# Performance work log

Hardware: AMD Instinct MI355X
Metric: run time of the kernel (lower is better)

Reference implementation:

```python
import jax, jax.numpy as jnp
import numpy as np

GAMMA = 0.99
NUM_QUANTILES = 50
STEP_TYPE_LAST = 2
HUBER_DELTA = 1.0

T, B, Q = 128, 512, NUM_QUANTILES


def setup_inputs() -> dict:
    key = jax.random.key(0)
    k1, k2, k3, k4, k5 = jax.random.split(key, 5)
    return {
        "reward": jax.random.normal(k1, (T, B), dtype=jnp.float32),
        "step_type": jax.random.randint(k2, (T, B), 0, 3, dtype=jnp.int32),
        "discount": jax.random.uniform(k3, (T, B), dtype=jnp.float32),
        "value": jax.random.normal(k4, (T, B, Q), dtype=jnp.float32),
        "target_value": jax.random.normal(k5, (T, B, Q), dtype=jnp.float32),
    }


def discounted_return(rewards, values, step_types, discounts):
    """alf value_ops.discounted_return: backward-in-time recurrence.

    rewards/step_types/discounts: [T, B]; values: [T, B, Q].
    Returns [T-1, B, Q]. rets[T-1]=values[T-1];
    rets[t] = is_last[t]*values[t] + (1-is_last[t])*(discounts[t+1]*rets[t+1] + rewards[t+1]).
    """
    is_last = (step_types == STEP_TYPE_LAST).astype(values.dtype)[..., None]  # [T,B,1]
    r = rewards[..., None]    # [T,B,1]
    d = discounts[..., None]  # [T,B,1]

    def step(carry, xs):
        is_last_t, v_t, r_tp1, d_tp1 = xs
        acc = carry * d_tp1 + r_tp1
        ret = is_last_t * v_t + (1.0 - is_last_t) * acc
        return ret, ret

    init = values[-1]
    xs = (is_last[:-1], values[:-1], r[1:], d[1:])
    _, rets = jax.lax.scan(step, init, xs, reverse=True)
    return rets  # [T-1, B, Q]


def huber(x):
    ax = jnp.abs(x)
    return jnp.where(ax <= HUBER_DELTA, 0.5 * x * x, HUBER_DELTA * (ax - 0.5 * HUBER_DELTA))


def reference(reward, step_type, discount, value, target_value):
    # td_lambda == 1.0 -> full discounted return (computed with no grad / detached)
    returns = jax.lax.stop_gradient(
        discounted_return(reward, target_value, step_type, discount * GAMMA))  # [T-1,B,Q]
    v = value[:-1]  # [T-1,B,Q]

    q = returns.shape[-1]
    tau = (jnp.arange(q, dtype=value.dtype) + 0.5) / q  # [Q] cdf midpoints

    # diff[..., i, j] = target_quantile_i - estimated_quantile_j
    diff = returns[..., :, None] - v[..., None, :]  # [T-1,B,Qt,Qe]
    weight = jnp.abs(tau - (jax.lax.stop_gradient(diff) < 0).astype(diff.dtype))
    loss = weight * huber(diff)
    # sum_over_quantiles=True: mean over target quantiles, sum over estimate quantiles
    loss = loss.mean(axis=-2).sum(axis=-1)  # [T-1,B]
    # tensor_extend_zero: append a zero row for the last time step -> [T,B]
    loss = jnp.concatenate([loss, jnp.zeros_like(loss[-1:])], axis=0)
    return loss
```

## Files before the change

kernel.cpp:

```cpp
#include <hip/hip_runtime.h>

#define GAMMA 0.99f
constexpr int T_DIM = 128;
constexpr int B_DIM = 512;
constexpr int Q_DIM = 50;
constexpr int TRET  = 127;
constexpr int SLOT  = 52;
constexpr int NSLOT = TRET * Q_DIM;
constexpr int KEEP  = -1;

__global__ void __launch_bounds__(1024) fused_kernel(
    const float* __restrict__ reward,
    const int*   __restrict__ step_type,
    const float* __restrict__ discount,
    const float* __restrict__ value,
    const float* __restrict__ tv,
    float*       __restrict__ out) {
  __shared__ __align__(16) float sret[TRET * SLOT];
  __shared__ float pacc[TRET * SLOT];
  __shared__ float sp[128], sqa[128], sqb[128];
  __shared__ int   snv[128];
  __shared__ float s_alpha[TRET], s_beta[TRET];
  __shared__ int   s_anchor[TRET];

  const int tid = threadIdx.x;
  const int b   = blockIdx.x;

  float p = 1.0f, qa = 0.0f, qb = 0.0f; int nv = KEEP;
  if (tid < TRET) {
    const bool  last = (step_type[tid * B_DIM + b] == 2);
    const float d    = GAMMA * discount[(tid + 1) * B_DIM + b];
    const float r    = reward[(tid + 1) * B_DIM + b];
    p  = last ? 0.0f : d;
    qa = last ? 1.0f : 0.0f;
    qb = last ? 0.0f : r;
    nv = last ? tid  : KEEP;
  } else if (tid == TRET) {
    out[TRET * B_DIM + b] = 0.0f;
  }
  if (tid < 128) { sp[tid] = p; sqa[tid] = qa; sqb[tid] = qb; snv[tid] = nv; }
  __syncthreads();

#pragma unroll
  for (int off = 1; off < 128; off <<= 1) {
    const bool act = (tid < 128) && (tid + off < 128);
    float p2 = 1.0f, qa2 = 0.0f, qb2 = 0.0f; int nv2 = KEEP;
    if (act) { p2 = sp[tid+off]; qa2 = sqa[tid+off]; qb2 = sqb[tid+off]; nv2 = snv[tid+off]; }
    __syncthreads();
    if (act) {
      qa = fmaf(p, qa2, qa);
      qb = fmaf(p, qb2, qb);
      p  = p * p2;
      nv = (nv == KEEP) ? nv2 : nv;
      sp[tid] = p; sqa[tid] = qa; sqb[tid] = qb; snv[tid] = nv;
    }
    __syncthreads();
  }

  if (tid < TRET) {
    s_alpha[tid]  = p + qa;
    s_beta[tid]   = qb;
    s_anchor[tid] = (nv == KEEP) ? TRET : nv;
  }
  __syncthreads();

  for (int e = tid; e < NSLOT; e += 1024) {
    const int t = e / Q_DIM;
    const int i = e - t * Q_DIM;
    const int n = s_anchor[t];
    sret[t * SLOT + i] =
        fmaf(s_alpha[t], tv[(n * B_DIM + b) * Q_DIM + i], s_beta[t]);
  }
  __syncthreads();

  for (int s = tid; s < NSLOT; s += 1024) {
    const int t = s / Q_DIM;
    const int j = s - t * Q_DIM;
    const float v    = value[(t * B_DIM + b) * Q_DIM + j];
    const float tm05 = ((float)j + 0.5f) * (1.0f / Q_DIM) - 0.5f;
    const float* rp  = &sret[t * SLOT];

    float s1 = 0.0f, s2 = 0.0f;
    auto pair = [&](float reti) {
      const float d = reti - v;
      const float c = __builtin_amdgcn_fmed3f(d, -1.0f, 1.0f);
      const float e = fmaf(-0.5f, c, d);
      s1 = fmaf(e, c, s1);
      s2 = fmaf(e, fabsf(c), s2);
    };
#pragma unroll
    for (int i0 = 0; i0 < 48; i0 += 4) {
      const float4 rr = *reinterpret_cast<const float4*>(rp + i0);
      pair(rr.x); pair(rr.y); pair(rr.z); pair(rr.w);
    }
    {
      const float2 rr = *reinterpret_cast<const float2*>(rp + 48);
      pair(rr.x); pair(rr.y);
    }
    pacc[t * SLOT + j] = fmaf(tm05, s2, 0.5f * s1);
  }
  __syncthreads();

  const int w    = tid >> 6;
  const int lane = tid & 63;
#pragma unroll
  for (int k = 0; k < 8; ++k) {
    const int t = w * 8 + k;
    if (t < TRET) {
      float x = (lane < Q_DIM) ? pacc[t * SLOT + lane] : 0.0f;
#pragma unroll
      for (int off = 32; off > 0; off >>= 1)
        x += __shfl_xor(x, off, 64);
      if (lane == 0) out[t * B_DIM + b] = x * (1.0f / Q_DIM);
    }
  }
}

extern "C" void kernel_launch(void* const* d_in, const int* in_sizes, int n_in,
                              void* d_out, int out_size, void* d_ws, size_t ws_size,
                              hipStream_t stream) {
  const float* reward       = (const float*)d_in[0];
  const int*   step_type    = (const int*)  d_in[1];
  const float* discount     = (const float*)d_in[2];
  const float* value        = (const float*)d_in[3];
  const float* target_value = (const float*)d_in[4];
  float* out = (float*)d_out;

  fused_kernel<<<B_DIM, 1024, 0, stream>>>(reward, step_type, discount,
                                           value, target_value, out);
}
```

Measured before the change: 102.0 us.

## Process two quantiles per thread, vectorize loads, double-buffer scan

Each thread now handles two estimate quantiles, so every shared-memory read of a return value feeds two pairwise Huber computations. Global loads of target_value and value become float2 loads. The prefix scan uses ping-pong buffers, which removes one barrier per step. Launch bounds ask for 8 waves per SIMD, which may constrain register allocation. The work split changes from 6350 items to 3175 pair items, which fit almost exactly into about 3 rounds of 1024 threads instead of about 7.

```diff
diff --git a/kernel.cpp b/kernel.cpp
--- a/kernel.cpp
+++ b/kernel.cpp
@@ -6,10 +6,10 @@
 constexpr int Q_DIM = 50;
 constexpr int TRET  = 127;
 constexpr int SLOT  = 52;
-constexpr int NSLOT = TRET * Q_DIM;
+constexpr int NPAIR = TRET * (Q_DIM/2);
 constexpr int KEEP  = -1;
 
-__global__ void __launch_bounds__(1024) fused_kernel(
+__global__ void __launch_bounds__(1024, 8) fused_kernel(
     const float* __restrict__ reward,
     const int*   __restrict__ step_type,
     const float* __restrict__ discount,
@@ -17,9 +17,9 @@
     const float* __restrict__ tv,
     float*       __restrict__ out) {
   __shared__ __align__(16) float sret[TRET * SLOT];
-  __shared__ float pacc[TRET * SLOT];
-  __shared__ float sp[128], sqa[128], sqb[128];
-  __shared__ int   snv[128];
+  __shared__ __align__(16) float pacc[TRET * SLOT];
+  __shared__ float sp[2][128], sqa[2][128], sqb[2][128];
+  __shared__ int   snv[2][128];
   __shared__ float s_alpha[TRET], s_beta[TRET];
   __shared__ int   s_anchor[TRET];
 
@@ -38,23 +38,30 @@
   } else if (tid == TRET) {
     out[TRET * B_DIM + b] = 0.0f;
   }
-  if (tid < 128) { sp[tid] = p; sqa[tid] = qa; sqb[tid] = qb; snv[tid] = nv; }
+  if (tid < 128) { sp[0][tid] = p; sqa[0][tid] = qa; sqb[0][tid] = qb; snv[0][tid] = nv; }
   __syncthreads();
 
+  int cur = 0;
 #pragma unroll
   for (int off = 1; off < 128; off <<= 1) {
-    const bool act = (tid < 128) && (tid + off < 128);
-    float p2 = 1.0f, qa2 = 0.0f, qb2 = 0.0f; int nv2 = KEEP;
-    if (act) { p2 = sp[tid+off]; qa2 = sqa[tid+off]; qb2 = sqb[tid+off]; nv2 = snv[tid+off]; }
-    __syncthreads();
-    if (act) {
-      qa = fmaf(p, qa2, qa);
-      qb = fmaf(p, qb2, qb);
-      p  = p * p2;
-      nv = (nv == KEEP) ? nv2 : nv;
-      sp[tid] = p; sqa[tid] = qa; sqb[tid] = qb; snv[tid] = nv;
+    if (tid < 128) {
+      if (tid + off < 128) {
+        const float p2  = sp [cur][tid + off];
+        const float qa2 = sqa[cur][tid + off];
+        const float qb2 = sqb[cur][tid + off];
+        const int   nv2 = snv[cur][tid + off];
+        qa = fmaf(p, qa2, qa);
+        qb = fmaf(p, qb2, qb);
+        p  = p * p2;
+        nv = (nv == KEEP) ? nv2 : nv;
+      }
+      sp [cur ^ 1][tid] = p;
+      sqa[cur ^ 1][tid] = qa;
+      sqb[cur ^ 1][tid] = qb;
+      snv[cur ^ 1][tid] = nv;
     }
     __syncthreads();
+    cur ^= 1;
   }
 
   if (tid < TRET) {
@@ -64,40 +71,52 @@
   }
   __syncthreads();
 
-  for (int e = tid; e < NSLOT; e += 1024) {
-    const int t = e / Q_DIM;
-    const int i = e - t * Q_DIM;
+  for (int e = tid; e < NPAIR; e += 1024) {
+    const int t = e / 25;
+    const int i = (e - t * 25) * 2;
     const int n = s_anchor[t];
-    sret[t * SLOT + i] =
-        fmaf(s_alpha[t], tv[(n * B_DIM + b) * Q_DIM + i], s_beta[t]);
+    const float  a  = s_alpha[t];
+    const float  be = s_beta[t];
+    const float2 tvv = *reinterpret_cast<const float2*>(
+        &tv[(n * B_DIM + b) * Q_DIM + i]);
+    *reinterpret_cast<float2*>(&sret[t * SLOT + i]) =
+        make_float2(fmaf(a, tvv.x, be), fmaf(a, tvv.y, be));
   }
   __syncthreads();
 
-  for (int s = tid; s < NSLOT; s += 1024) {
-    const int t = s / Q_DIM;
-    const int j = s - t * Q_DIM;
-    const float v    = value[(t * B_DIM + b) * Q_DIM + j];
-    const float tm05 = ((float)j + 0.5f) * (1.0f / Q_DIM) - 0.5f;
-    const float* rp  = &sret[t * SLOT];
+  for (int s = tid; s < NPAIR; s += 1024) {
+    const int t  = s / 25;
+    const int j0 = (s - t * 25) * 2;
+    const float2 vv = *reinterpret_cast<const float2*>(
+        &value[(t * B_DIM + b) * Q_DIM + j0]);
+    const float ta0 = ((float)j0 + 0.5f) * (1.0f / Q_DIM) - 0.5f;
+    const float ta1 = ((float)j0 + 1.5f) * (1.0f / Q_DIM) - 0.5f;
+    const float* rp = &sret[t * SLOT];
 
-    float s1 = 0.0f, s2 = 0.0f;
-    auto pair = [&](float reti) {
-      const float d = reti - v;
-      const float c = __builtin_amdgcn_fmed3f(d, -1.0f, 1.0f);
-      const float e = fmaf(-0.5f, c, d);
-      s1 = fmaf(e, c, s1);
-      s2 = fmaf(e, fabsf(c), s2);
+    float s1a = 0.0f, s2a = 0.0f, s1b = 0.0f, s2b = 0.0f;
+    auto pair2 = [&](float reti) {
+      { const float d = reti - vv.x;
+        const float c = __builtin_amdgcn_fmed3f(d, -1.0f, 1.0f);
+        const float e = fmaf(-0.5f, c, d);
+        s1a = fmaf(e, c, s1a);
+        s2a = fmaf(e, fabsf(c), s2a); }
+      { const float d = reti - vv.y;
+        const float c = __builtin_amdgcn_fmed3f(d, -1.0f, 1.0f);
+        const float e = fmaf(-0.5f, c, d);
+        s1b = fmaf(e, c, s1b);
+        s2b = fmaf(e, fabsf(c), s2b); }
     };
 #pragma unroll
     for (int i0 = 0; i0 < 48; i0 += 4) {
       const float4 rr = *reinterpret_cast<const float4*>(rp + i0);
-      pair(rr.x); pair(rr.y); pair(rr.z); pair(rr.w);
+      pair2(rr.x); pair2(rr.y); pair2(rr.z); pair2(rr.w);
     }
     {
       const float2 rr = *reinterpret_cast<const float2*>(rp + 48);
-      pair(rr.x); pair(rr.y);
+      pair2(rr.x); pair2(rr.y);
     }
-    pacc[t * SLOT + j] = fmaf(tm05, s2, 0.5f * s1);
+    *reinterpret_cast<float2*>(&pacc[t * SLOT + j0]) =
+        make_float2(fmaf(ta0, s2a, 0.5f * s1a), fmaf(ta1, s2b, 0.5f * s1b));
   }
   __syncthreads();
 
```

Measured after the change: 103.3 us. No clear change (+1.2%).
